# Performance work log

Measured on AMD Instinct MI355X. Metric: run time of the kernel, lower is better.

## Reference

```python
import jax, jax.numpy as jnp
import numpy as np

NUM_EMBEDDINGS = 1024
EMBEDDING_DIM = 256
BETA = 0.25


def setup_inputs() -> dict:
    key = jax.random.key(0)
    k1, k2 = jax.random.split(key)
    z = jax.random.normal(k1, (32, EMBEDDING_DIM, 32, 32), dtype=jnp.float32)
    lim = 1.0 / NUM_EMBEDDINGS
    embedding = jax.random.uniform(k2, (NUM_EMBEDDINGS, EMBEDDING_DIM),
                                   dtype=jnp.float32, minval=-lim, maxval=lim)
    return {"z": z, "embedding": embedding}


def reference(z, embedding):
    # NCHW -> NHWC, flatten to [N, D]
    z_nhwc = jnp.transpose(z, (0, 2, 3, 1))
    B, H, W, D = z_nhwc.shape
    z_flat = z_nhwc.reshape(-1, D)  # [N, D]

    # squared L2 distances: ||z||^2 + ||e||^2 - 2 z e^T  -> [N, K]
    dists = (jnp.sum(z_flat ** 2, axis=1, keepdims=True)
             + jnp.sum(embedding ** 2, axis=1)
             - 2.0 * jnp.matmul(z_flat, embedding.T))

    idx = jnp.argmin(dists, axis=1)  # [N]
    min_encodings = jax.nn.one_hot(idx, NUM_EMBEDDINGS, dtype=jnp.float32)  # [N, K]

    # gather nearest codebook vectors (== matmul(one_hot, embedding))
    z_q = embedding[idx].reshape(B, H, W, D)

    # commitment + codebook loss
    loss = (jnp.mean((jax.lax.stop_gradient(z_q) - z_nhwc) ** 2)
            + BETA * jnp.mean((z_q - jax.lax.stop_gradient(z_nhwc)) ** 2))

    # straight-through estimator
    z_q = z_nhwc + jax.lax.stop_gradient(z_q - z_nhwc)
    z_q = jnp.transpose(z_q, (0, 3, 1, 2))  # NHWC -> NCHW

    return (loss, z_q, min_encodings, idx)
```

## Files before the change

### kernel.cpp

```cpp
#include <hip/hip_runtime.h>
#include <math.h>

#define DIM   256
#define NUM_E 1024
#define HWN   1024
#define NROW  32768
#define NELEM 8388608

#define BM 128
#define BN 128
#define BK 32
#define NCH 8

__device__ __forceinline__ float np_sumsq_128(const float* __restrict__ a,
                                              int stride) {
#pragma clang fp contract(off)
    float r[8];
#pragma unroll
    for (int j = 0; j < 8; ++j) { const float v = a[j * stride]; r[j] = v * v; }
    for (int i = 8; i < 128; i += 8) {
#pragma unroll
        for (int j = 0; j < 8; ++j) {
            const float v = a[(i + j) * stride];
            r[j] += v * v;
        }
    }
    return ((r[0] + r[1]) + (r[2] + r[3])) + ((r[4] + r[5]) + (r[6] + r[7]));
}

__global__ __launch_bounds__(256) void k_pre(const float* __restrict__ z,
                                             const float* __restrict__ emb,
                                             float* __restrict__ zz,
                                             float* __restrict__ ee) {
    const int g = blockIdx.x * 256 + threadIdx.x;
    if (blockIdx.x < 256) {
        const int r = g >> 1, hh = g & 1;
        const int b = r >> 10, hw = r & (HWN - 1);
        const float h = np_sumsq_128(
            z + (size_t)b * DIM * HWN + (size_t)(hh * 128) * HWN + hw, HWN);
        const float o = __shfl_down(h, 1, 64);
        if (!hh) zz[r] = h + o;
    } else {
        const int ge = g - 65536;
        const int k = ge >> 1, hh = ge & 1;
        const float h = np_sumsq_128(emb + (size_t)k * DIM + hh * 128, 1);
        const float o = __shfl_down(h, 1, 64);
        if (!hh) ee[k] = h + o;
    }
}

__global__ __launch_bounds__(256, 4) void k_gemm(
        const float* __restrict__ z, const float* __restrict__ emb,
        const float* __restrict__ zzg, const float* __restrict__ eeg,
        float* __restrict__ cv, int* __restrict__ ci) {
    __shared__ __align__(16) float zs[BK * BM];
    __shared__ __align__(16) float es[BK * BN];
    float4* zs4 = (float4*)zs;
    float4* es4 = (float4*)es;

    const int tid = threadIdx.x;
    const int nb  = blockIdx.x & (NCH - 1);
    const int mb  = blockIdx.x >> 3;
    const int R0  = mb * BM;
    const int b   = R0 >> 10;
    const int hw0 = R0 & (HWN - 1);

    const int tx = tid & 15, ty = tid >> 4;
    const int kg = tid & 7, ng = tid >> 3;
    const int wslot = ng ^ kg;
    const int m4 = tid & 31, kzb = tid >> 5;

    const float* zbase = z + (size_t)b * DIM * HWN + hw0;
    const float4* embq = (const float4*)(emb + ((size_t)nb * BN + ng * 4) * DIM);

    float acc[8][8];
#pragma unroll
    for (int i = 0; i < 8; ++i)
#pragma unroll
        for (int j = 0; j < 8; ++j) acc[i][j] = 0.f;

    for (int k0 = 0; k0 < DIM; k0 += BK) {
        __syncthreads();
#pragma unroll
        for (int q = 0; q < 4; ++q) {
            const int k = q * 8 + kzb;
            zs4[k * 32 + m4] =
                *(const float4*)(zbase + (size_t)(k0 + k) * HWN + m4 * 4);
        }
        {
            const float4 g0 = embq[0 * 64 + (k0 >> 2) + kg];
            const float4 g1 = embq[1 * 64 + (k0 >> 2) + kg];
            const float4 g2 = embq[2 * 64 + (k0 >> 2) + kg];
            const float4 g3 = embq[3 * 64 + (k0 >> 2) + kg];
            es4[(kg * 4 + 0) * 32 + wslot] = make_float4(g0.x, g1.x, g2.x, g3.x);
            es4[(kg * 4 + 1) * 32 + wslot] = make_float4(g0.y, g1.y, g2.y, g3.y);
            es4[(kg * 4 + 2) * 32 + wslot] = make_float4(g0.z, g1.z, g2.z, g3.z);
            es4[(kg * 4 + 3) * 32 + wslot] = make_float4(g0.w, g1.w, g2.w, g3.w);
        }
        __syncthreads();

#pragma unroll
        for (int k4 = 0; k4 < 8; ++k4) {
            const int sA = tx ^ k4;
            const int sB = sA + 16;
#pragma unroll
            for (int kj = 0; kj < 4; ++kj) {
                const int k = k4 * 4 + kj;
                const float4 za0 = zs4[k * 32 + ty * 2];
                const float4 za1 = zs4[k * 32 + ty * 2 + 1];
                const float4 eb0 = es4[k * 32 + sA];
                const float4 eb1 = es4[k * 32 + sB];
                const float zf[8] = {za0.x, za0.y, za0.z, za0.w,
                                     za1.x, za1.y, za1.z, za1.w};
                const float ef[8] = {eb0.x, eb0.y, eb0.z, eb0.w,
                                     eb1.x, eb1.y, eb1.z, eb1.w};
#pragma unroll
                for (int i = 0; i < 8; ++i)
#pragma unroll
                    for (int j = 0; j < 8; ++j)
                        acc[i][j] = fmaf(zf[i], ef[j], acc[i][j]);
            }
        }
    }

    const int n0a = nb * BN + tx * 4;
    const int n0b = n0a + 64;
#pragma unroll
    for (int i = 0; i < 8; ++i) {
        const int r = R0 + ty * 8 + i;
        const float zzv = zzg[r];
        float bv = 1e30f; int bi = 0;
#pragma unroll
        for (int j = 0; j < 8; ++j) {
            const int kk = (j < 4) ? (n0a + j) : (n0b + j - 4);
            const float t    = zzv + eeg[kk];
            const float dist = t - 2.0f * acc[i][j];
            if (dist < bv) { bv = dist; bi = kk; }
        }
#pragma unroll
        for (int off = 1; off <= 8; off <<= 1) {
            const float v2 = __shfl_xor(bv, off, 64);
            const int   i2 = __shfl_xor(bi, off, 64);
            if (v2 < bv || (v2 == bv && i2 < bi)) { bv = v2; bi = i2; }
        }
        if (tx == 0) {
            cv[(size_t)nb * NROW + r] = bv;
            ci[(size_t)nb * NROW + r] = bi;
        }
    }
}

__global__ __launch_bounds__(256) void k_amfin(const float* __restrict__ cv,
                                               const int* __restrict__ ci,
                                               float* __restrict__ oidx) {
    const int r = blockIdx.x * 256 + threadIdx.x;
    float bv = cv[r]; int bi = ci[r];
#pragma unroll
    for (int c = 1; c < NCH; ++c) {
        const float v = cv[(size_t)c * NROW + r];
        const int   x = ci[(size_t)c * NROW + r];
        if (v < bv || (v == bv && x < bi)) { bv = v; bi = x; }
    }
    oidx[r] = (float)bi;
}

__global__ __launch_bounds__(256) void k_onehot(const float* __restrict__ idxf,
                                                float4* __restrict__ enc4) {
    const int t = threadIdx.x;
#pragma unroll
    for (int i = 0; i < 16; ++i) {
        const int row = blockIdx.x * 16 + i;
        const int k = (int)idxf[row];
        float4 v = make_float4(0.f, 0.f, 0.f, 0.f);
        if ((k >> 2) == t) ((float*)&v)[k & 3] = 1.0f;
        enc4[(size_t)row * 256 + t] = v;
    }
}

__global__ __launch_bounds__(256) void k_zq(const float* __restrict__ z,
                                            const float* __restrict__ emb,
                                            const float* __restrict__ idxf,
                                            float* __restrict__ ozq,
                                            double* __restrict__ partials) {
    const int gid = blockIdx.x * 256 + threadIdx.x;
    const int hw4 = gid & 255;
    const int d   = (gid >> 8) & 255;
    const int b   = gid >> 16;
    const size_t zoff = ((size_t)(b * DIM + d)) * HWN + hw4 * 4;
    const float4 zv = *(const float4*)(z + zoff);
    const int n0 = b * HWN + hw4 * 4;
    const int i0 = (int)idxf[n0 + 0], i1 = (int)idxf[n0 + 1];
    const int i2 = (int)idxf[n0 + 2], i3 = (int)idxf[n0 + 3];
    const float e0 = emb[i0 * DIM + d], e1 = emb[i1 * DIM + d];
    const float e2 = emb[i2 * DIM + d], e3 = emb[i3 * DIM + d];
    const float t0 = e0 - zv.x, t1 = e1 - zv.y, t2 = e2 - zv.z, t3 = e3 - zv.w;
    const float4 o = make_float4(zv.x + t0, zv.y + t1, zv.z + t2, zv.w + t3);
    *(float4*)(ozq + zoff) = o;
    double s = (double)t0 * t0 + (double)t1 * t1 + (double)t2 * t2 + (double)t3 * t3;
#pragma unroll
    for (int off = 32; off > 0; off >>= 1) s += __shfl_down(s, off, 64);
    __shared__ double pw[4];
    if ((threadIdx.x & 63) == 0) pw[threadIdx.x >> 6] = s;
    __syncthreads();
    if (threadIdx.x == 0)
        partials[blockIdx.x] = (pw[0] + pw[1]) + (pw[2] + pw[3]);
}

__global__ __launch_bounds__(256) void k_fin(const double* __restrict__ partials,
                                             float* __restrict__ out) {
    const int t = threadIdx.x;
    double s = 0.0;
    for (int i = t; i < 8192; i += 256) s += partials[i];
#pragma unroll
    for (int off = 32; off > 0; off >>= 1) s += __shfl_down(s, off, 64);
    __shared__ double w[4];
    if ((t & 63) == 0) w[t >> 6] = s;
    __syncthreads();
    if (t == 0) {
        const double tot = (w[0] + w[1]) + (w[2] + w[3]);
        const float m = (float)(tot / 8388608.0);
        out[0] = m + 0.25f * m;
    }
}

extern "C" void kernel_launch(void* const* d_in, const int* in_sizes, int n_in,
                              void* d_out, int out_size, void* d_ws, size_t ws_size,
                              hipStream_t stream) {
    const float* z   = (const float*)d_in[0];
    const float* emb = (const float*)d_in[1];
    float* out   = (float*)d_out;
    float* o_zq  = out + 1;
    float* o_enc = o_zq + NELEM;
    float* o_idx = o_enc + (size_t)NROW * NUM_E;

    float*  s_cv = o_enc;
    int*    s_ci = (int*)(o_enc + 262144);
    float*  s_zz = o_enc + 524288;
    float*  s_ee = o_enc + 557056;
    double* s_ps = (double*)(((size_t)(o_enc + 600000) + 7) & ~(size_t)7);

    k_pre   <<<264, 256, 0, stream>>>(z, emb, s_zz, s_ee);
    k_gemm  <<<(NROW / BM) * NCH, 256, 0, stream>>>(z, emb, s_zz, s_ee, s_cv, s_ci);
    k_amfin <<<NROW / 256, 256, 0, stream>>>(s_cv, s_ci, o_idx);
    k_zq    <<<NELEM / 4 / 256, 256, 0, stream>>>(z, emb, o_idx, o_zq, s_ps);
    k_fin   <<<1, 256, 0, stream>>>(s_ps, out);
    k_onehot<<<NROW / 16, 256, 0, stream>>>(o_idx, (float4*)o_enc);
}
```

Before: 448.0 us.

## Prefetch GEMM tiles in registers, fuse argmin with one-hot, use workspace scratch

The GEMM kernel now loads the next K-slice of z and the codebook into registers while the current tile is computed, overlapping global loads with FMA work, and its occupancy hint drops from 4 to 3 blocks to leave room for the extra registers. When workspace is large enough, scratch buffers move out of the one-hot output region into d_ws. That allows the cross-chunk argmin reduction to be fused with the one-hot write, which now uses branchless vector nontemporal stores. The final loss reduction uses 1024 threads. The fused kernel recomputes the argmin in every thread, and the lower occupancy may hide latency less well.

```diff
diff --git a/kernel.cpp b/kernel.cpp
--- a/kernel.cpp
+++ b/kernel.cpp
@@ -11,6 +11,8 @@
 #define BN 128
 #define BK 32
 #define NCH 8
+
+typedef float f32x4 __attribute__((ext_vector_type(4)));
 
 __device__ __forceinline__ float np_sumsq_128(const float* __restrict__ a,
                                               int stride) {
@@ -49,7 +51,7 @@
     }
 }
 
-__global__ __launch_bounds__(256, 4) void k_gemm(
+__global__ __launch_bounds__(256, 3) void k_gemm(
         const float* __restrict__ z, const float* __restrict__ emb,
         const float* __restrict__ zzg, const float* __restrict__ eeg,
         float* __restrict__ cv, int* __restrict__ ci) {
@@ -79,25 +81,34 @@
 #pragma unroll
         for (int j = 0; j < 8; ++j) acc[i][j] = 0.f;
 
-    for (int k0 = 0; k0 < DIM; k0 += BK) {
+    float4 pz[4], pe[4];
+#pragma unroll
+    for (int q = 0; q < 4; ++q)
+        pz[q] = *(const float4*)(zbase + (size_t)(q * 8 + kzb) * HWN + m4 * 4);
+#pragma unroll
+    for (int i = 0; i < 4; ++i)
+        pe[i] = embq[(size_t)i * 64 + kg];
+
+    for (int t8 = 0; t8 < 8; ++t8) {
         __syncthreads();
 #pragma unroll
-        for (int q = 0; q < 4; ++q) {
-            const int k = q * 8 + kzb;
-            zs4[k * 32 + m4] =
-                *(const float4*)(zbase + (size_t)(k0 + k) * HWN + m4 * 4);
-        }
-        {
-            const float4 g0 = embq[0 * 64 + (k0 >> 2) + kg];
-            const float4 g1 = embq[1 * 64 + (k0 >> 2) + kg];
-            const float4 g2 = embq[2 * 64 + (k0 >> 2) + kg];
-            const float4 g3 = embq[3 * 64 + (k0 >> 2) + kg];
-            es4[(kg * 4 + 0) * 32 + wslot] = make_float4(g0.x, g1.x, g2.x, g3.x);
-            es4[(kg * 4 + 1) * 32 + wslot] = make_float4(g0.y, g1.y, g2.y, g3.y);
-            es4[(kg * 4 + 2) * 32 + wslot] = make_float4(g0.z, g1.z, g2.z, g3.z);
-            es4[(kg * 4 + 3) * 32 + wslot] = make_float4(g0.w, g1.w, g2.w, g3.w);
-        }
+        for (int q = 0; q < 4; ++q)
+            zs4[(q * 8 + kzb) * 32 + m4] = pz[q];
+        es4[(kg * 4 + 0) * 32 + wslot] = make_float4(pe[0].x, pe[1].x, pe[2].x, pe[3].x);
+        es4[(kg * 4 + 1) * 32 + wslot] = make_float4(pe[0].y, pe[1].y, pe[2].y, pe[3].y);
+        es4[(kg * 4 + 2) * 32 + wslot] = make_float4(pe[0].z, pe[1].z, pe[2].z, pe[3].z);
+        es4[(kg * 4 + 3) * 32 + wslot] = make_float4(pe[0].w, pe[1].w, pe[2].w, pe[3].w);
         __syncthreads();
+
+        if (t8 < 7) {
+            const int k0n = (t8 + 1) * BK;
+#pragma unroll
+            for (int q = 0; q < 4; ++q)
+                pz[q] = *(const float4*)(zbase + (size_t)(k0n + q * 8 + kzb) * HWN + m4 * 4);
+#pragma unroll
+            for (int i = 0; i < 4; ++i)
+                pe[i] = embq[(size_t)i * 64 + (k0n >> 2) + kg];
+        }
 
 #pragma unroll
         for (int k4 = 0; k4 < 8; ++k4) {
@@ -150,6 +161,31 @@
     }
 }
 
+__global__ __launch_bounds__(256) void k_ohid(const float* __restrict__ cv,
+                                              const int* __restrict__ ci,
+                                              float* __restrict__ oidx,
+                                              f32x4* __restrict__ enc4) {
+    const int t = threadIdx.x;
+#pragma unroll 4
+    for (int i = 0; i < 16; ++i) {
+        const int row = blockIdx.x * 16 + i;
+        float bv = cv[row]; int bi = ci[row];
+#pragma unroll
+        for (int c = 1; c < NCH; ++c) {
+            const float v = cv[(size_t)c * NROW + row];
+            const int   x = ci[(size_t)c * NROW + row];
+            if (v < bv || (v == bv && x < bi)) { bv = v; bi = x; }
+        }
+        if (t == 0) oidx[row] = (float)bi;
+        const int k0 = t * 4;
+        const f32x4 v4 = {bi == k0     ? 1.f : 0.f,
+                          bi == k0 + 1 ? 1.f : 0.f,
+                          bi == k0 + 2 ? 1.f : 0.f,
+                          bi == k0 + 3 ? 1.f : 0.f};
+        __builtin_nontemporal_store(v4, &enc4[(size_t)row * 256 + t]);
+    }
+}
+
 __global__ __launch_bounds__(256) void k_amfin(const float* __restrict__ cv,
                                                const int* __restrict__ ci,
                                                float* __restrict__ oidx) {
@@ -165,15 +201,18 @@
 }
 
 __global__ __launch_bounds__(256) void k_onehot(const float* __restrict__ idxf,
-                                                float4* __restrict__ enc4) {
+                                                f32x4* __restrict__ enc4) {
     const int t = threadIdx.x;
-#pragma unroll
+#pragma unroll 4
     for (int i = 0; i < 16; ++i) {
         const int row = blockIdx.x * 16 + i;
         const int k = (int)idxf[row];
-        float4 v = make_float4(0.f, 0.f, 0.f, 0.f);
-        if ((k >> 2) == t) ((float*)&v)[k & 3] = 1.0f;
-        enc4[(size_t)row * 256 + t] = v;
+        const int k0 = t * 4;
+        const f32x4 v4 = {k == k0     ? 1.f : 0.f,
+                          k == k0 + 1 ? 1.f : 0.f,
+                          k == k0 + 2 ? 1.f : 0.f,
+                          k == k0 + 3 ? 1.f : 0.f};
+        __builtin_nontemporal_store(v4, &enc4[(size_t)row * 256 + t]);
     }
 }
 
@@ -206,18 +245,21 @@
         partials[blockIdx.x] = (pw[0] + pw[1]) + (pw[2] + pw[3]);
 }
 
-__global__ __launch_bounds__(256) void k_fin(const double* __restrict__ partials,
-                                             float* __restrict__ out) {
+__global__ __launch_bounds__(1024) void k_fin(const double* __restrict__ partials,
+                                              float* __restrict__ out) {
     const int t = threadIdx.x;
     double s = 0.0;
-    for (int i = t; i < 8192; i += 256) s += partials[i];
+#pragma unroll
+    for (int i = 0; i < 8; ++i) s += partials[t + i * 1024];
 #pragma unroll
     for (int off = 32; off > 0; off >>= 1) s += __shfl_down(s, off, 64);
-    __shared__ double w[4];
+    __shared__ double w[16];
     if ((t & 63) == 0) w[t >> 6] = s;
     __syncthreads();
     if (t == 0) {
-        const double tot = (w[0] + w[1]) + (w[2] + w[3]);
+        double tot = 0.0;
+#pragma unroll
+        for (int i = 0; i < 16; ++i) tot += w[i];
         const float m = (float)(tot / 8388608.0);
         out[0] = m + 0.25f * m;
     }
@@ -233,16 +275,33 @@
     float* o_enc = o_zq + NELEM;
     float* o_idx = o_enc + (size_t)NROW * NUM_E;
 
-    float*  s_cv = o_enc;
-    int*    s_ci = (int*)(o_enc + 262144);
-    float*  s_zz = o_enc + 524288;
-    float*  s_ee = o_enc + 557056;
-    double* s_ps = (double*)(((size_t)(o_enc + 600000) + 7) & ~(size_t)7);
-
-    k_pre   <<<264, 256, 0, stream>>>(z, emb, s_zz, s_ee);
-    k_gemm  <<<(NROW / BM) * NCH, 256, 0, stream>>>(z, emb, s_zz, s_ee, s_cv, s_ci);
-    k_amfin <<<NROW / 256, 256, 0, stream>>>(s_cv, s_ci, o_idx);
-    k_zq    <<<NELEM / 4 / 256, 256, 0, stream>>>(z, emb, o_idx, o_zq, s_ps);
-    k_fin   <<<1, 256, 0, stream>>>(s_ps, out);
-    k_onehot<<<NROW / 16, 256, 0, stream>>>(o_idx, (float4*)o_enc);
-}
+    const size_t need_bytes = (size_t)(262144 + 262144 + 32768 + 1024) * 4
+                            + (size_t)8192 * 8 + 64;
+
+    if (ws_size >= need_bytes) {
+        float*  s_cv = (float*)d_ws;
+        int*    s_ci = (int*)(s_cv + 262144);
+        float*  s_zz = (float*)(s_ci + 262144);
+        float*  s_ee = s_zz + 32768;
+        double* s_ps = (double*)(s_ee + 1024);
+
+        k_pre  <<<264, 256, 0, stream>>>(z, emb, s_zz, s_ee);
+        k_gemm <<<(NROW / BM) * NCH, 256, 0, stream>>>(z, emb, s_zz, s_ee, s_cv, s_ci);
+        k_ohid <<<NROW / 16, 256, 0, stream>>>(s_cv, s_ci, o_idx, (f32x4*)o_enc);
+        k_zq   <<<NELEM / 4 / 256, 256, 0, stream>>>(z, emb, o_idx, o_zq, s_ps);
+        k_fin  <<<1, 1024, 0, stream>>>(s_ps, out);
+    } else {
+        float*  s_cv = o_enc;
+        int*    s_ci = (int*)(o_enc + 262144);
+        float*  s_zz = o_enc + 524288;
+        float*  s_ee = o_enc + 557056;
+        double* s_ps = (double*)(((size_t)(o_enc + 600000) + 7) & ~(size_t)7);
+
+        k_pre   <<<264, 256, 0, stream>>>(z, emb, s_zz, s_ee);
+        k_gemm  <<<(NROW / BM) * NCH, 256, 0, stream>>>(z, emb, s_zz, s_ee, s_cv, s_ci);
+        k_amfin <<<NROW / 256, 256, 0, stream>>>(s_cv, s_ci, o_idx);
+        k_zq    <<<NELEM / 4 / 256, 256, 0, stream>>>(z, emb, o_idx, o_zq, s_ps);
+        k_fin   <<<1, 1024, 0, stream>>>(s_ps, out);
+        k_onehot<<<NROW / 16, 256, 0, stream>>>(o_idx, (f32x4*)o_enc);
+    }
+}
```

After: 477.4 us. 6.6% more time.
